# Kernel optimization log

Measured on AMD Instinct MI355X. Metric: run time of the kernel, lower is better.

## Reference

```python
import jax, jax.numpy as jnp
import numpy as np

N0, N1, N2 = 50000, 12500, 3125
E0, E1, E2 = 800000, 200000, 50000
NNZ = 200000          # nonzeros per interpolation matrix (~4 per fine node)
H = 128               # hidden_channels
F = 32                # feat_dim
L = 3                 # layers
DEC_W = 64            # decoder width


def setup_inputs() -> dict:
    key = jax.random.key(0)
    ks = iter(jax.random.split(key, 64))
    f32 = jnp.float32
    d = {}
    # node features per level
    d['x0'] = jax.random.normal(next(ks), (N0, 6), f32)
    d['x1'] = jax.random.normal(next(ks), (N1, 6), f32)
    d['x2'] = jax.random.normal(next(ks), (N2, 6), f32)
    # edge lists per level
    d['edge_index0'] = jax.random.randint(next(ks), (2, E0), 0, N0)
    d['edge_index1'] = jax.random.randint(next(ks), (2, E1), 0, N1)
    d['edge_index2'] = jax.random.randint(next(ks), (2, E2), 0, N2)
    # sparse interpolation matrices A1: [N0,N1], A2: [N0,N2] in COO
    d['A1_rows'] = jax.random.randint(next(ks), (NNZ,), 0, N0)
    d['A1_cols'] = jax.random.randint(next(ks), (NNZ,), 0, N1)
    d['A1_vals'] = jax.random.uniform(next(ks), (NNZ,), f32)
    d['A2_rows'] = jax.random.randint(next(ks), (NNZ,), 0, N0)
    d['A2_cols'] = jax.random.randint(next(ks), (NNZ,), 0, N2)
    d['A2_vals'] = jax.random.uniform(next(ks), (NNZ,), f32)
    # encoder params, stacked over L layers. GraphConv: lin_rel (bias) + lin_root (no bias)
    s = 0.05
    d['enc_c1_Wrel'] = jax.random.normal(next(ks), (L, 6, H), f32) * s
    d['enc_c1_brel'] = jnp.zeros((L, H), f32)
    d['enc_c1_Wroot'] = jax.random.normal(next(ks), (L, 6, H), f32) * s
    d['enc_c2_Wrel'] = jax.random.normal(next(ks), (L, H, H), f32) * s
    d['enc_c2_brel'] = jnp.zeros((L, H), f32)
    d['enc_c2_Wroot'] = jax.random.normal(next(ks), (L, H, H), f32) * s
    d['enc_lin_W'] = jax.random.normal(next(ks), (L, H, 3 * F), f32) * s
    d['enc_lin_b'] = jnp.zeros((L, 3 * F), f32)
    # decoder params (D=1, W=64, in=L*F, out=1), stacked over 3 decoders
    d['dec_W0'] = jax.random.normal(next(ks), (3, L * F, DEC_W), f32) * s
    d['dec_b0'] = jnp.zeros((3, DEC_W), f32)
    d['dec_Wout'] = jax.random.normal(next(ks), (3, DEC_W, 1), f32) * s
    d['dec_bout'] = jnp.zeros((3, 1), f32)
    return d


def _graph_conv(x, src, dst, Wrel, brel, Wroot, n):
    # PyG GraphConv: lin_rel(sum_{j->i} x_j) + lin_root(x_i)
    agg = jax.ops.segment_sum(x[src], dst, num_segments=n)
    return agg @ Wrel + brel + x @ Wroot


def reference(x0, x1, x2, edge_index0, edge_index1, edge_index2,
              A1_rows, A1_cols, A1_vals, A2_rows, A2_cols, A2_vals,
              enc_c1_Wrel, enc_c1_brel, enc_c1_Wroot,
              enc_c2_Wrel, enc_c2_brel, enc_c2_Wroot,
              enc_lin_W, enc_lin_b,
              dec_W0, dec_b0, dec_Wout, dec_bout):
    xs = (x0, x1, x2)
    eis = (edge_index0, edge_index1, edge_index2)

    def enc(i):
        x, ei = xs[i], eis[i]
        n = x.shape[0]
        src, dst = ei[0], ei[1]
        h = jax.nn.relu(_graph_conv(x, src, dst, enc_c1_Wrel[i], enc_c1_brel[i], enc_c1_Wroot[i], n))
        h = jax.nn.relu(_graph_conv(h, src, dst, enc_c2_Wrel[i], enc_c2_brel[i], enc_c2_Wroot[i], n))
        return h @ enc_lin_W[i] + enc_lin_b[i]  # [n, 3*F]

    e0 = enc(0).reshape(N0, 3, F)
    e1 = enc(1)  # [N1, 3F]
    e2 = enc(2)  # [N2, 3F]
    # sparse.mm(A, dense) as gather-scale-scatter
    i1 = jax.ops.segment_sum(A1_vals[:, None] * e1[A1_cols], A1_rows, num_segments=N0).reshape(N0, 3, F)
    i2 = jax.ops.segment_sum(A2_vals[:, None] * e2[A2_cols], A2_rows, num_segments=N0).reshape(N0, 3, F)
    interped = jnp.concatenate([e0, i1, i2], axis=2)  # [N0, 3, L*F]

    def dec(i):
        h = interped[:, i:i + 1, :]                       # [N0, 1, L*F]
        h = jax.nn.elu(h @ dec_W0[i] + dec_b0[i])         # [N0, 1, 64]
        return h @ dec_Wout[i] + dec_bout[i]              # [N0, 1, 1]

    return jnp.concatenate([dec(0), dec(1), dec(2)], axis=1)  # [N0, 3, 1]
```

## Files before the change

### kernel.cpp

```cpp
#include <hip/hip_runtime.h>
#include <math.h>

#define N0 50000
#define N1 12500
#define N2 3125
#define NNZ 200000
#define NE0 800000
#define NE1 200000
#define NE2 50000
#define NT 65625
#define SEG_TOT 165625
#define EDGE_TOT 1050000
#define ITEM_TOT 1450000
#define NBUCK 324
#define SPB 512
#define NBLK 355

typedef __attribute__((ext_vector_type(8))) short short8;
typedef __attribute__((ext_vector_type(8))) unsigned short ushort8;
typedef __attribute__((ext_vector_type(4))) float floatx4;

__device__ inline void split_bf16(float x, unsigned short& hi, unsigned short& lo) {
    unsigned xb = __float_as_uint(x);
    hi = (unsigned short)(xb >> 16);
    float hf = __uint_as_float((unsigned)hi << 16);
    lo = (unsigned short)(__float_as_uint(x - hf) >> 16);
}

__device__ inline void split8(const float* p, short8& hi, short8& lo) {
    float4 u0 = *(const float4*)p;
    float4 u1 = *(const float4*)(p + 4);
    float f[8] = {u0.x, u0.y, u0.z, u0.w, u1.x, u1.y, u1.z, u1.w};
#pragma unroll
    for (int j = 0; j < 8; j++) {
        unsigned short h, l;
        split_bf16(f[j], h, l);
        hi[j] = (short)h; lo[j] = (short)l;
    }
}


__device__ inline int item_seg(int t, const int* __restrict__ ei0,
                               const int* __restrict__ ei1, const int* __restrict__ ei2,
                               const int* __restrict__ A1r, const int* __restrict__ A2r) {
    if (t < NE0) return ei0[NE0 + t];
    if (t < NE0 + NE1) return 50000 + ei1[NE1 + (t - NE0)];
    if (t < EDGE_TOT) return 62500 + ei2[NE2 + (t - (NE0 + NE1))];
    if (t < EDGE_TOT + NNZ) return NT + A1r[t - EDGE_TOT];
    return NT + N0 + A2r[t - (EDGE_TOT + NNZ)];
}

__global__ __launch_bounds__(256) void bin_hist(const int* __restrict__ ei0,
        const int* __restrict__ ei1, const int* __restrict__ ei2,
        const int* __restrict__ A1r, const int* __restrict__ A2r,
        int* __restrict__ hist_g, int* __restrict__ btot) {
    __shared__ int h[NBUCK];
    for (int i = threadIdx.x; i < NBUCK; i += 256) h[i] = 0;
    __syncthreads();
    int base = blockIdx.x * 4096;
#pragma unroll
    for (int q = 0; q < 16; q++) {
        int t = base + q * 256 + threadIdx.x;
        if (t < ITEM_TOT) atomicAdd(&h[item_seg(t, ei0, ei1, ei2, A1r, A2r) >> 9], 1);
    }
    __syncthreads();
    for (int i = threadIdx.x; i < NBUCK; i += 256) {
        int v = h[i];
        hist_g[i * NBLK + blockIdx.x] = v;
        if (v) atomicAdd(&btot[i], v);
    }
}

__global__ void hist_scan(int* __restrict__ hist_g, const int* __restrict__ btot,
                          int* __restrict__ bbase) {
    int b = blockIdx.x, lane = threadIdx.x;
    int s = 0;
    for (int j = lane; j < b; j += 64) s += btot[j];
#pragma unroll
    for (int o = 32; o > 0; o >>= 1) s += __shfl_down(s, o, 64);
    int base = __shfl(s, 0, 64);
    if (lane == 0) {
        bbase[b] = base;
        if (b == NBUCK - 1) bbase[NBUCK] = ITEM_TOT;
    }
    int v[6], ts = 0;
#pragma unroll
    for (int q = 0; q < 6; q++) {
        int i = lane * 6 + q;
        v[q] = (i < NBLK) ? hist_g[b * NBLK + i] : 0;
        ts += v[q];
    }
    int sc = ts;
#pragma unroll
    for (int o = 1; o < 64; o <<= 1) {
        int t2 = __shfl_up(sc, o, 64);
        if (lane >= o) sc += t2;
    }
    int run = base + sc - ts;
#pragma unroll
    for (int q = 0; q < 6; q++) {
        int i = lane * 6 + q;
        if (i < NBLK) hist_g[b * NBLK + i] = run;
        run += v[q];
    }
}

__global__ __launch_bounds__(256) void bin_scatter(const int* __restrict__ ei0,
        const int* __restrict__ ei1, const int* __restrict__ ei2,
        const int* __restrict__ A1r, const int* __restrict__ A1c, const float* __restrict__ A1v,
        const int* __restrict__ A2r, const int* __restrict__ A2c, const float* __restrict__ A2v,
        const int* __restrict__ hist_g, int* __restrict__ bpacked, float* __restrict__ bval) {
    __shared__ int cur[NBUCK];
    for (int i = threadIdx.x; i < NBUCK; i += 256) cur[i] = hist_g[i * NBLK + blockIdx.x];
    __syncthreads();
    int base = blockIdx.x * 4096;
#pragma unroll
    for (int q = 0; q < 16; q++) {
        int t = base + q * 256 + threadIdx.x;
        if (t >= ITEM_TOT) continue;
        int seg, pay;
        float val = 0.f;
        bool isv = false;
        if (t < NE0) { seg = ei0[NE0 + t]; pay = ei0[t]; }
        else if (t < NE0 + NE1) { int e = t - NE0; seg = 50000 + ei1[NE1 + e]; pay = ei1[e]; }
        else if (t < EDGE_TOT) { int e = t - (NE0 + NE1); seg = 62500 + ei2[NE2 + e]; pay = ei2[e]; }
        else if (t < EDGE_TOT + NNZ) { int k = t - EDGE_TOT; seg = NT + A1r[k]; pay = A1c[k]; val = A1v[k]; isv = true; }
        else { int k = t - (EDGE_TOT + NNZ); seg = NT + N0 + A2r[k]; pay = A2c[k]; val = A2v[k]; isv = true; }
        int bk = seg >> 9;
        int p = atomicAdd(&cur[bk], 1);
        bpacked[p] = ((seg - (bk << 9)) << 16) | pay;
        if (isv) bval[p] = val;
    }
}

__global__ __launch_bounds__(256) void bucket_fill(const int* __restrict__ bpacked,
        const float* __restrict__ bval, const int* __restrict__ bbase,
        int* __restrict__ offs, int* __restrict__ csrc, float* __restrict__ cval) {
    __shared__ int cnt[SPB];
    __shared__ int wsum2[4];
    int b = blockIdx.x, tid = threadIdx.x;
    int segbase = b * SPB;
    int seglim = SEG_TOT - segbase;
    if (seglim > SPB) seglim = SPB;
    int ibeg = bbase[b], iend = bbase[b + 1];
    for (int i = tid; i < SPB; i += 256) cnt[i] = 0;
    __syncthreads();
    for (int i = ibeg + tid; i < iend; i += 256)
        atomicAdd(&cnt[bpacked[i] >> 16], 1);
    __syncthreads();
    int lane = tid & 63, wid = tid >> 6;
    int v0 = cnt[tid * 2], v1 = cnt[tid * 2 + 1];
    int ts = v0 + v1, sc = ts;
#pragma unroll
    for (int o = 1; o < 64; o <<= 1) {
        int t2 = __shfl_up(sc, o, 64);
        if (lane >= o) sc += t2;
    }
    if (lane == 63) wsum2[wid] = sc;
    __syncthreads();
    int woff = 0;
    for (int w = 0; w < wid; w++) woff += wsum2[w];
    int ex = ibeg + woff + sc - ts;
    __syncthreads();
    cnt[tid * 2] = ex;
    cnt[tid * 2 + 1] = ex + v0;
    if (tid * 2 < seglim) offs[segbase + tid * 2] = ex;
    if (tid * 2 + 1 < seglim) offs[segbase + tid * 2 + 1] = ex + v0;
    if (b == NBUCK - 1 && tid == 0) offs[SEG_TOT] = ITEM_TOT;
    __syncthreads();
    for (int i = ibeg + tid; i < iend; i += 256) {
        int w2 = bpacked[i];
        int sl = w2 >> 16, pay = w2 & 0xffff;
        int p = atomicAdd(&cnt[sl], 1);
        csrc[p] = pay;
        if (segbase + sl >= NT) cval[p - EDGE_TOT] = bval[i];
    }
}


__device__ inline void acc_u4(uint4 u, float* a) {
    a[0] += __uint_as_float(u.x << 16);
    a[1] += __uint_as_float(u.x & 0xffff0000u);
    a[2] += __uint_as_float(u.y << 16);
    a[3] += __uint_as_float(u.y & 0xffff0000u);
    a[4] += __uint_as_float(u.z << 16);
    a[5] += __uint_as_float(u.z & 0xffff0000u);
    a[6] += __uint_as_float(u.w << 16);
    a[7] += __uint_as_float(u.w & 0xffff0000u);
}

__global__ __launch_bounds__(256) void gatherH_b(const unsigned short* __restrict__ h1hi,
                                                 const int* __restrict__ offs,
                                                 const int* __restrict__ csrc,
                                                 float* __restrict__ agg) {
    int t = blockIdx.x * blockDim.x + threadIdx.x;
    int n = t >> 4, g = t & 15;
    if (n >= NT) return;
    int nb = (n < 50000) ? 0 : (n < 62500 ? 50000 : 62500);
    float a[8] = {};
    int b = offs[n], e = offs[n + 1];
    int j = b;
    for (; j + 3 < e; j += 4) {
        int s0 = csrc[j], s1 = csrc[j + 1], s2 = csrc[j + 2], s3 = csrc[j + 3];
        uint4 u0 = *(const uint4*)(h1hi + (size_t)(nb + s0) * 128 + g * 8);
        uint4 u1 = *(const uint4*)(h1hi + (size_t)(nb + s1) * 128 + g * 8);
        uint4 u2 = *(const uint4*)(h1hi + (size_t)(nb + s2) * 128 + g * 8);
        uint4 u3 = *(const uint4*)(h1hi + (size_t)(nb + s3) * 128 + g * 8);
        acc_u4(u0, a);
        acc_u4(u1, a);
        acc_u4(u2, a);
        acc_u4(u3, a);
    }
    for (; j < e; j++) {
        uint4 u0 = *(const uint4*)(h1hi + (size_t)(nb + csrc[j]) * 128 + g * 8);
        acc_u4(u0, a);
    }
    float* o = agg + (size_t)n * 128 + g * 8;
    *(float4*)o = (float4){a[0], a[1], a[2], a[3]};
    *(float4*)(o + 4) = (float4){a[4], a[5], a[6], a[7]};
}

__global__ __launch_bounds__(256) void interp_b(const float* __restrict__ ecat,
                                                const int* __restrict__ offs,
                                                const int* __restrict__ csrc,
                                                const float* __restrict__ cval,
                                                float* __restrict__ i1, float* __restrict__ i2) {
    int t = blockIdx.x * blockDim.x + threadIdx.x;
    int ng = t / 24, g = t % 24;
    if (ng >= 2 * N0) return;
    int a = (ng >= N0) ? 1 : 0;
    int nl = ng - a * N0;
    const float* e = ecat + (size_t)(a ? 62500 : 50000) * 96;
    float* ob = a ? i2 : i1;
    int seg = NT + ng;
    float4 s = {0.f, 0.f, 0.f, 0.f};
    int b = offs[seg], en = offs[seg + 1];
    int j = b;
    for (; j + 1 < en; j += 2) {
        int c0 = csrc[j], c1 = csrc[j + 1];
        float v0 = cval[j - EDGE_TOT], v1 = cval[j + 1 - EDGE_TOT];
        float4 w0 = ((const float4*)(e + (size_t)c0 * 96))[g];
        float4 w1 = ((const float4*)(e + (size_t)c1 * 96))[g];
        s.x += v0 * w0.x + v1 * w1.x;
        s.y += v0 * w0.y + v1 * w1.y;
        s.z += v0 * w0.z + v1 * w1.z;
        s.w += v0 * w0.w + v1 * w1.w;
    }
    if (j < en) {
        int c0 = csrc[j];
        float v0 = cval[j - EDGE_TOT];
        float4 w0 = ((const float4*)(e + (size_t)c0 * 96))[g];
        s.x += v0 * w0.x; s.y += v0 * w0.y; s.z += v0 * w0.z; s.w += v0 * w0.w;
    }
    ((float4*)(ob + (size_t)nl * 96))[g] = s;
}

__global__ void conv_weights(const float* __restrict__ c2Wrel, const float* __restrict__ c2Wroot,
                             const float* __restrict__ linW, const float* __restrict__ dW0,
                             unsigned short* __restrict__ c2hi, unsigned short* __restrict__ c2lo,
                             unsigned short* __restrict__ lhi, unsigned short* __restrict__ llo,
                             float* __restrict__ decWt, int* __restrict__ btot) {
    int t = blockIdx.x * blockDim.x + threadIdx.x;
    if (t <= NBUCK) btot[t] = 0;
    if (t < 98304) {
        int i = t / 32768, r = t % 32768;
        int n = r / 256, k = r % 256;
        float w = (k < 128) ? c2Wrel[i * 16384 + k * 128 + n]
                            : c2Wroot[i * 16384 + (k - 128) * 128 + n];
        unsigned short hi, lo;
        split_bf16(w, hi, lo);
        c2hi[t] = hi; c2lo[t] = lo;
    } else if (t < 135168) {
        int u = t - 98304;
        int i = u / 12288, r = u % 12288;
        int n = r / 128, k = r % 128;
        unsigned short hi, lo;
        split_bf16(linW[i * 12288 + k * 96 + n], hi, lo);
        lhi[u] = hi; llo[u] = lo;
    } else if (t < 153600) {
        int u = t - 135168;
        int chn = u / 6144, r = u % 6144;
        int col = r / 96, k = r % 96;
        decWt[u] = dW0[chn * 6144 + k * 64 + col];
    }
}

__global__ __launch_bounds__(256) void conv1_b(
        const int* __restrict__ offs, const int* __restrict__ csrc,
        const float* __restrict__ x0, const float* __restrict__ x1,
        const float* __restrict__ x2,
        const float* __restrict__ Wrel, const float* __restrict__ Wroot,
        const float* __restrict__ brel,
        unsigned short* __restrict__ h1hi, unsigned short* __restrict__ h1lo) {
    __shared__ float As[12][65];
    __shared__ float Ws[12][64];
    int bx = blockIdx.x;
    int l, lbk;
    if (bx < 782) { l = 0; lbk = bx; }
    else if (bx < 978) { l = 1; lbk = bx - 782; }
    else { l = 2; lbk = bx - 978; }
    int nb = (l == 0) ? 0 : (l == 1 ? 50000 : 62500);
    int M = (l == 0) ? N0 : (l == 1 ? N1 : N2);
    const float* xl = (l == 0) ? x0 : (l == 1 ? x1 : x2);
    const float* W1 = Wrel + l * 768;
    const float* W2 = Wroot + l * 768;
    const float* bias = brel + l * 128;
    int m0 = lbk * 64, n0 = blockIdx.y * 64;
    int tid = threadIdx.x;

    {
        int row = tid >> 2, sub = tid & 3;
        int m = m0 + row;
        float a6[6] = {};
        if (m < M) {
            int jb = offs[nb + m], je = offs[nb + m + 1];
            for (int j = jb + sub; j < je; j += 4) {
                const float* p = xl + (size_t)csrc[j] * 6;
                a6[0] += p[0]; a6[1] += p[1]; a6[2] += p[2];
                a6[3] += p[3]; a6[4] += p[4]; a6[5] += p[5];
            }
        }
#pragma unroll
        for (int msk = 1; msk < 4; msk <<= 1) {
#pragma unroll
            for (int q = 0; q < 6; q++) a6[q] += __shfl_xor(a6[q], msk, 64);
        }
        if (sub == 0) {
#pragma unroll
            for (int q = 0; q < 6; q++) As[q][row] = (m < M) ? a6[q] : 0.f;
        } else if (sub == 1) {
#pragma unroll
            for (int q = 0; q < 6; q++)
                As[6 + q][row] = (m < M) ? xl[(size_t)m * 6 + q] : 0.f;
        }
    }
    for (int idx = tid; idx < 768; idx += 256) {
        int kk = idx >> 6, nn2 = idx & 63;
        Ws[kk][nn2] = (kk < 6) ? W1[kk * 128 + n0 + nn2] : W2[(kk - 6) * 128 + n0 + nn2];
    }
    __syncthreads();

    int tm = tid >> 4, tn = tid & 15;
    float acc[4][4] = {};
#pragma unroll
    for (int k = 0; k < 12; k++) {
        float av[4], wv[4];
#pragma unroll
        for (int i = 0; i < 4; i++) av[i] = As[k][tm * 4 + i];
#pragma unroll
        for (int j = 0; j < 4; j++) wv[j] = Ws[k][tn * 4 + j];
#pragma unroll
        for (int i = 0; i < 4; i++)
#pragma unroll
            for (int j = 0; j < 4; j++) acc[i][j] += av[i] * wv[j];
    }
#pragma unroll
    for (int i = 0; i < 4; i++) {
        int m = m0 + tm * 4 + i;
        if (m >= M) continue;
        unsigned short hs[4], ls[4];
#pragma unroll
        for (int j = 0; j < 4; j++) {
            float v = fmaxf(acc[i][j] + bias[n0 + tn * 4 + j], 0.f);
            split_bf16(v, hs[j], ls[j]);
        }
        uint2 ph = {(unsigned)hs[0] | ((unsigned)hs[1] << 16),
                    (unsigned)hs[2] | ((unsigned)hs[3] << 16)};
        uint2 pl = {(unsigned)ls[0] | ((unsigned)ls[1] << 16),
                    (unsigned)ls[2] | ((unsigned)ls[3] << 16)};
        size_t off = (size_t)(nb + m) * 128 + n0 + tn * 4;
        *(uint2*)(h1hi + off) = ph;
        *(uint2*)(h1lo + off) = pl;
    }
}

__global__ __launch_bounds__(256) void conv2lin(
        const float* __restrict__ agg,
        const unsigned short* __restrict__ h1hi, const unsigned short* __restrict__ h1lo,
        const unsigned short* __restrict__ c2hi, const unsigned short* __restrict__ c2lo,
        const float* __restrict__ c2b,
        const unsigned short* __restrict__ lnhi, const unsigned short* __restrict__ lnlo,
        const float* __restrict__ lnb, float* __restrict__ ecat) {
    __shared__ unsigned short smem[25088];
    unsigned short* Ah = smem;
    unsigned short* Al = smem + 2560;
    unsigned short* Bh = smem + 5120;
    unsigned short* Bl = smem + 10240;
    unsigned short* Hh = smem;
    unsigned short* Hl = smem + 8704;
    unsigned short* B2h = smem + 17408;
    unsigned short* B2l = smem + 21248;
    const int LDA = 40;

    int bx = blockIdx.x;
    int l, lbk;
    if (bx < 782) { l = 0; lbk = bx; }
    else if (bx < 978) { l = 1; lbk = bx - 782; }
    else { l = 2; lbk = bx - 978; }
    int nb = (l == 0) ? 0 : (l == 1 ? 50000 : 62500);
    int M = (l == 0) ? N0 : (l == 1 ? N1 : N2);
    const float* A1 = agg + (size_t)nb * 128;
    const unsigned short* A2h = h1hi + (size_t)nb * 128;
    const unsigned short* A2l = h1lo + (size_t)nb * 128;
    const unsigned short* W1h = c2hi + l * 32768;
    const unsigned short* W1l = c2lo + l * 32768;
    const float* b1 = c2b + l * 128;
    const unsigned short* W2h = lnhi + l * 12288;
    const unsigned short* W2l = lnlo + l * 12288;
    const float* b2 = lnb + l * 96;
    float* C = ecat + (size_t)nb * 96;
    int m0 = lbk * 64;

    int tid = threadIdx.x;
    int lane = tid & 63, wid = tid >> 6;
    int waveM = wid & 1, waveN = wid >> 1;
    int l15 = lane & 15, quad = lane >> 4;
    int arow = tid >> 2, acol = (tid & 3) * 8;
    int brow = tid >> 1, bcol = (tid & 1) * 16;

    floatx4 acc[2][4];
#pragma unroll
    for (int i = 0; i < 2; i++)
#pragma unroll
        for (int j = 0; j < 4; j++) acc[i][j] = (floatx4){0.f, 0.f, 0.f, 0.f};

    for (int kt = 0; kt < 256; kt += 32) {
        __syncthreads();
        {
            int m = m0 + arow;
            ushort8 hv, lv;
            if (m < M) {
                int kg = kt + acol;
                if (kg < 128) {
                    const float* src = A1 + (size_t)m * 128 + kg;
                    float4 u0 = *(const float4*)src;
                    float4 u1 = *(const float4*)(src + 4);
                    float xv[8] = {u0.x, u0.y, u0.z, u0.w, u1.x, u1.y, u1.z, u1.w};
#pragma unroll
                    for (int q = 0; q < 8; q++) {
                        unsigned short h, lo2;
                        split_bf16(xv[q], h, lo2);
                        hv[q] = h; lv[q] = lo2;
                    }
                } else {
                    size_t off = (size_t)m * 128 + (kg - 128);
                    hv = *(const ushort8*)(A2h + off);
                    lv = *(const ushort8*)(A2l + off);
                }
            } else {
                hv = (ushort8)0; lv = (ushort8)0;
            }
            *(ushort8*)(&Ah[arow * LDA + acol]) = hv;
            *(ushort8*)(&Al[arow * LDA + acol]) = lv;
        }
        {
            const unsigned short* ph = W1h + (size_t)brow * 256 + kt + bcol;
            const unsigned short* pl = W1l + (size_t)brow * 256 + kt + bcol;
            *(ushort8*)(&Bh[brow * LDA + bcol]) = *(const ushort8*)ph;
            *(ushort8*)(&Bh[brow * LDA + bcol + 8]) = *(const ushort8*)(ph + 8);
            *(ushort8*)(&Bl[brow * LDA + bcol]) = *(const ushort8*)pl;
            *(ushort8*)(&Bl[brow * LDA + bcol + 8]) = *(const ushort8*)(pl + 8);
        }
        __syncthreads();
        short8 af[2][2];
#pragma unroll
        for (int mt = 0; mt < 2; mt++) {
            int r = waveM * 32 + mt * 16 + l15;
            af[mt][0] = *(const short8*)(&Ah[r * LDA + quad * 8]);
            af[mt][1] = *(const short8*)(&Al[r * LDA + quad * 8]);
        }
#pragma unroll
        for (int nt = 0; nt < 4; nt++) {
            int c = waveN * 64 + nt * 16 + l15;
            short8 bh = *(const short8*)(&Bh[c * LDA + quad * 8]);
            short8 bl = *(const short8*)(&Bl[c * LDA + quad * 8]);
#pragma unroll
            for (int mt = 0; mt < 2; mt++) {
                acc[mt][nt] = __builtin_amdgcn_mfma_f32_16x16x32_bf16(af[mt][0], bh, acc[mt][nt], 0, 0, 0);
                acc[mt][nt] = __builtin_amdgcn_mfma_f32_16x16x32_bf16(af[mt][0], bl, acc[mt][nt], 0, 0, 0);
                acc[mt][nt] = __builtin_amdgcn_mfma_f32_16x16x32_bf16(af[mt][1], bh, acc[mt][nt], 0, 0, 0);
            }
        }
    }

    __syncthreads();
    {
        float bs1[4];
#pragma unroll
        for (int nt = 0; nt < 4; nt++) bs1[nt] = b1[waveN * 64 + nt * 16 + l15];
#pragma unroll
        for (int mt = 0; mt < 2; mt++)
#pragma unroll
            for (int nt = 0; nt < 4; nt++)
#pragma unroll
                for (int r = 0; r < 4; r++) {
                    int row = waveM * 32 + mt * 16 + quad * 4 + r;
                    int col = waveN * 64 + nt * 16 + l15;
                    float v = fmaxf(acc[mt][nt][r] + bs1[nt], 0.f);
                    unsigned short h, lo2;
                    split_bf16(v, h, lo2);
                    Hh[row * 136 + col] = h;
                    Hl[row * 136 + col] = lo2;
                }
    }

    floatx4 acc2[2][3];
#pragma unroll
    for (int i = 0; i < 2; i++)
#pragma unroll
        for (int j = 0; j < 3; j++) acc2[i][j] = (floatx4){0.f, 0.f, 0.f, 0.f};

    for (int kt = 0; kt < 128; kt += 32) {
        __syncthreads();
        if (brow < 96) {
            const unsigned short* ph = W2h + (size_t)brow * 128 + kt + bcol;
            const unsigned short* pl = W2l + (size_t)brow * 128 + kt + bcol;
            *(ushort8*)(&B2h[brow * LDA + bcol]) = *(const ushort8*)ph;
            *(ushort8*)(&B2h[brow * LDA + bcol + 8]) = *(const ushort8*)(ph + 8);
            *(ushort8*)(&B2l[brow * LDA + bcol]) = *(const ushort8*)pl;
            *(ushort8*)(&B2l[brow * LDA + bcol + 8]) = *(const ushort8*)(pl + 8);
        }
        __syncthreads();
        short8 af2[2][2];
#pragma unroll
        for (int mt = 0; mt < 2; mt++) {
            int r = waveM * 32 + mt * 16 + l15;
            af2[mt][0] = *(const short8*)(&Hh[r * 136 + kt + quad * 8]);
            af2[mt][1] = *(const short8*)(&Hl[r * 136 + kt + quad * 8]);
        }
#pragma unroll
        for (int nt = 0; nt < 3; nt++) {
            int c = waveN * 48 + nt * 16 + l15;
            short8 bh = *(const short8*)(&B2h[c * LDA + quad * 8]);
            short8 bl = *(const short8*)(&B2l[c * LDA + quad * 8]);
#pragma unroll
            for (int mt = 0; mt < 2; mt++) {
                acc2[mt][nt] = __builtin_amdgcn_mfma_f32_16x16x32_bf16(af2[mt][0], bh, acc2[mt][nt], 0, 0, 0);
                acc2[mt][nt] = __builtin_amdgcn_mfma_f32_16x16x32_bf16(af2[mt][0], bl, acc2[mt][nt], 0, 0, 0);
                acc2[mt][nt] = __builtin_amdgcn_mfma_f32_16x16x32_bf16(af2[mt][1], bh, acc2[mt][nt], 0, 0, 0);
            }
        }
    }

    float bs2[3];
#pragma unroll
    for (int nt = 0; nt < 3; nt++) bs2[nt] = b2[waveN * 48 + nt * 16 + l15];
#pragma unroll
    for (int mt = 0; mt < 2; mt++)
#pragma unroll
        for (int r = 0; r < 4; r++) {
            int grow = m0 + waveM * 32 + mt * 16 + quad * 4 + r;
            if (grow >= M) continue;
#pragma unroll
            for (int nt = 0; nt < 3; nt++) {
                int col = waveN * 48 + nt * 16 + l15;
                C[(size_t)grow * 96 + col] = acc2[mt][nt][r] + bs2[nt];
            }
        }
}

__global__ __launch_bounds__(256) void decoder_mfma(
        const float* __restrict__ e0, const float* __restrict__ i1,
        const float* __restrict__ i2, const float* __restrict__ decWt,
        const float* __restrict__ b0, const float* __restrict__ Wout,
        const float* __restrict__ bout, float* __restrict__ out, int N) {
    __shared__ float As[6400];
    __shared__ float Bs[6400];
    __shared__ float red[64][2];
    __shared__ float sb0[64], sWo[64];
    int ch = blockIdx.y;
    int tid = threadIdx.x;
    int m0 = blockIdx.x * 64;

    for (int idx = tid; idx < 1536; idx += 256) {
        int col = idx / 24, k0 = (idx % 24) * 4;
        *(float4*)(&Bs[col * 100 + k0]) = *(const float4*)(decWt + ch * 6144 + col * 96 + k0);
    }
    if (tid < 64) { sb0[tid] = b0[ch * 64 + tid]; sWo[tid] = Wout[ch * 64 + tid]; }
    for (int idx = tid; idx < 1536; idx += 256) {
        int row = idx / 24, k0 = (idx % 24) * 4;
        int m = m0 + row;
        float4 v = {0.f, 0.f, 0.f, 0.f};
        if (m < N) {
            const float* base = (k0 < 32) ? e0 : (k0 < 64 ? i1 : i2);
            v = *(const float4*)(base + (size_t)m * 96 + ch * 32 + (k0 & 31));
        }
        *(float4*)(&As[row * 100 + k0]) = v;
    }
    __syncthreads();

    int lane = tid & 63, wid = tid >> 6;
    int waveM = wid & 1, waveN = wid >> 1;
    int l15 = lane & 15, quad = lane >> 4;
    floatx4 acc[2][2];
#pragma unroll
    for (int i = 0; i < 2; i++)
#pragma unroll
        for (int j = 0; j < 2; j++) acc[i][j] = (floatx4){0.f, 0.f, 0.f, 0.f};

#pragma unroll
    for (int kt = 0; kt < 96; kt += 32) {
        short8 ah[2], al[2];
#pragma unroll
        for (int mt = 0; mt < 2; mt++) {
            int r = waveM * 32 + mt * 16 + l15;
            split8(&As[r * 100 + kt + quad * 8], ah[mt], al[mt]);
        }
#pragma unroll
        for (int nt = 0; nt < 2; nt++) {
            int c = waveN * 32 + nt * 16 + l15;
            short8 bh, bl;
            split8(&Bs[c * 100 + kt + quad * 8], bh, bl);
#pragma unroll
            for (int mt = 0; mt < 2; mt++) {
                acc[mt][nt] = __builtin_amdgcn_mfma_f32_16x16x32_bf16(ah[mt], bh, acc[mt][nt], 0, 0, 0);
                acc[mt][nt] = __builtin_amdgcn_mfma_f32_16x16x32_bf16(ah[mt], bl, acc[mt][nt], 0, 0, 0);
                acc[mt][nt] = __builtin_amdgcn_mfma_f32_16x16x32_bf16(al[mt], bh, acc[mt][nt], 0, 0, 0);
            }
        }
    }

    float cb0[2], cwo[2];
#pragma unroll
    for (int nt = 0; nt < 2; nt++) {
        int col = waveN * 32 + nt * 16 + l15;
        cb0[nt] = sb0[col]; cwo[nt] = sWo[col];
    }
    float p[2][4];
#pragma unroll
    for (int mt = 0; mt < 2; mt++)
#pragma unroll
        for (int r = 0; r < 4; r++) {
            float s = 0.f;
#pragma unroll
            for (int nt = 0; nt < 2; nt++) {
                float h = acc[mt][nt][r] + cb0[nt];
                h = h > 0.f ? h : (expf(h) - 1.0f);
                s += h * cwo[nt];
            }
            p[mt][r] = s;
        }
#pragma unroll
    for (int mt = 0; mt < 2; mt++)
#pragma unroll
        for (int r = 0; r < 4; r++) {
#pragma unroll
            for (int msk = 1; msk < 16; msk <<= 1)
                p[mt][r] += __shfl_xor(p[mt][r], msk, 64);
        }
    if (l15 == 0) {
#pragma unroll
        for (int mt = 0; mt < 2; mt++)
#pragma unroll
            for (int r = 0; r < 4; r++) {
                int row = waveM * 32 + mt * 16 + quad * 4 + r;
                red[row][waveN] = p[mt][r];
            }
    }
    __syncthreads();
    if (tid < 64) {
        int m = m0 + tid;
        if (m < N) out[(size_t)m * 3 + ch] = red[tid][0] + red[tid][1] + bout[ch];
    }
}


extern "C" void kernel_launch(void* const* d_in, const int* in_sizes, int n_in,
                              void* d_out, int out_size, void* d_ws, size_t ws_size,
                              hipStream_t stream) {
    const float* x0 = (const float*)d_in[0];
    const float* x1 = (const float*)d_in[1];
    const float* x2 = (const float*)d_in[2];
    const int* ei0 = (const int*)d_in[3];
    const int* ei1 = (const int*)d_in[4];
    const int* ei2 = (const int*)d_in[5];
    const int* A1r = (const int*)d_in[6];
    const int* A1c = (const int*)d_in[7];
    const float* A1v = (const float*)d_in[8];
    const int* A2r = (const int*)d_in[9];
    const int* A2c = (const int*)d_in[10];
    const float* A2v = (const float*)d_in[11];
    const float* c1Wrel = (const float*)d_in[12];
    const float* c1brel = (const float*)d_in[13];
    const float* c1Wroot = (const float*)d_in[14];
    const float* c2Wrel = (const float*)d_in[15];
    const float* c2brel = (const float*)d_in[16];
    const float* c2Wroot = (const float*)d_in[17];
    const float* linW = (const float*)d_in[18];
    const float* linb = (const float*)d_in[19];
    const float* dW0 = (const float*)d_in[20];
    const float* db0 = (const float*)d_in[21];
    const float* dWout = (const float*)d_in[22];
    const float* dbout = (const float*)d_in[23];
    float* out = (float*)d_out;

    float* ws = (float*)d_ws;
    unsigned short* h1hi = (unsigned short*)(ws + 400000);
    unsigned short* h1lo = (unsigned short*)(ws + 4600000);
    float* aggH = ws + 8800000;
    float* ecat = ws + 17200000;
    int* bpacked = (int*)(ws + 8800000);
    float* bval = ws + 8800000 + 1450000;
    float* i1 = aggH;
    float* i2 = ws + 400000;
    int* hist_g = (int*)(ws + 23500000);
    int* btot = (int*)(ws + 23615020);
    int* bbase = (int*)(ws + 23615344);
    int* offs = (int*)(ws + 23665632);
    int* csrc = (int*)(ws + 23831264);
    float* cval = ws + 25281392;
    unsigned short* c2hi = (unsigned short*)(ws + 25681392);
    unsigned short* c2lo = c2hi + 98304;
    unsigned short* lnhi = c2lo + 98304;
    unsigned short* lnlo = lnhi + 36864;
    float* decWt = ws + 25681392 + 135168;

    conv_weights<<<(153600 + 255) / 256, 256, 0, stream>>>(
        c2Wrel, c2Wroot, linW, dW0, c2hi, c2lo, lnhi, lnlo, decWt, btot);

    bin_hist<<<NBLK, 256, 0, stream>>>(ei0, ei1, ei2, A1r, A2r, hist_g, btot);
    hist_scan<<<NBUCK, 64, 0, stream>>>(hist_g, btot, bbase);
    bin_scatter<<<NBLK, 256, 0, stream>>>(ei0, ei1, ei2, A1r, A1c, A1v,
                                          A2r, A2c, A2v, hist_g, bpacked, bval);
    bucket_fill<<<NBUCK, 256, 0, stream>>>(bpacked, bval, bbase, offs, csrc, cval);

    dim3 g1(1027, 2);
    conv1_b<<<g1, 256, 0, stream>>>(offs, csrc, x0, x1, x2,
                                    c1Wrel, c1Wroot, c1brel, h1hi, h1lo);
    gatherH_b<<<((size_t)NT * 16 + 255) / 256, 256, 0, stream>>>(h1hi, offs, csrc, aggH);
    conv2lin<<<1027, 256, 0, stream>>>(aggH, h1hi, h1lo, c2hi, c2lo, c2brel,
                                       lnhi, lnlo, linb, ecat);

    interp_b<<<((size_t)2 * N0 * 24 + 255) / 256, 256, 0, stream>>>(
        ecat, offs, csrc, cval, i1, i2);

    dim3 gd(782, 3);
    decoder_mfma<<<gd, 256, 0, stream>>>(ecat, i1, i2, decWt, db0, dWout, dbout, out, N0);
}
```

Measured before the change: 306.5 us.

## Store aggregated conv2 input as single bf16 and merge conv1 column blocks

The neighbor aggregate of conv1 output is now written as round-to-nearest bf16 instead of fp32. This halves its write and read traffic, and conv2lin drops the lo-part split and its MFMA for the first half of K. conv1_b now computes all 128 output columns per block instead of launching two column blocks, so the neighbor gather of x runs once rather than twice. Workspace offsets are shuffled so the bucket buffers no longer alias the aggregate. The trade is reduced precision on the aggregated term of the second conv.

```diff
diff --git a/kernel.cpp b/kernel.cpp
--- a/kernel.cpp
+++ b/kernel.cpp
@@ -25,6 +25,11 @@
     hi = (unsigned short)(xb >> 16);
     float hf = __uint_as_float((unsigned)hi << 16);
     lo = (unsigned short)(__float_as_uint(x - hf) >> 16);
+}
+
+__device__ inline unsigned short bf16_rne(float x) {
+    unsigned xb = __float_as_uint(x);
+    return (unsigned short)((xb + 0x7fff + ((xb >> 16) & 1)) >> 16);
 }
 
 __device__ inline void split8(const float* p, short8& hi, short8& lo) {
@@ -192,7 +197,7 @@
 __global__ __launch_bounds__(256) void gatherH_b(const unsigned short* __restrict__ h1hi,
                                                  const int* __restrict__ offs,
                                                  const int* __restrict__ csrc,
-                                                 float* __restrict__ agg) {
+                                                 unsigned short* __restrict__ aggh) {
     int t = blockIdx.x * blockDim.x + threadIdx.x;
     int n = t >> 4, g = t & 15;
     if (n >= NT) return;
@@ -215,9 +220,10 @@
         uint4 u0 = *(const uint4*)(h1hi + (size_t)(nb + csrc[j]) * 128 + g * 8);
         acc_u4(u0, a);
     }
-    float* o = agg + (size_t)n * 128 + g * 8;
-    *(float4*)o = (float4){a[0], a[1], a[2], a[3]};
-    *(float4*)(o + 4) = (float4){a[4], a[5], a[6], a[7]};
+    ushort8 o;
+#pragma unroll
+    for (int q = 0; q < 8; q++) o[q] = bf16_rne(a[q]);
+    *(ushort8*)(aggh + (size_t)n * 128 + g * 8) = o;
 }
 
 __global__ __launch_bounds__(256) void interp_b(const float* __restrict__ ecat,
@@ -293,7 +299,7 @@
         const float* __restrict__ brel,
         unsigned short* __restrict__ h1hi, unsigned short* __restrict__ h1lo) {
     __shared__ float As[12][65];
-    __shared__ float Ws[12][64];
+    __shared__ float Ws[12][128];
     int bx = blockIdx.x;
     int l, lbk;
     if (bx < 782) { l = 0; lbk = bx; }
@@ -305,7 +311,7 @@
     const float* W1 = Wrel + l * 768;
     const float* W2 = Wroot + l * 768;
     const float* bias = brel + l * 128;
-    int m0 = lbk * 64, n0 = blockIdx.y * 64;
+    int m0 = lbk * 64;
     int tid = threadIdx.x;
 
     {
@@ -334,48 +340,52 @@
                 As[6 + q][row] = (m < M) ? xl[(size_t)m * 6 + q] : 0.f;
         }
     }
-    for (int idx = tid; idx < 768; idx += 256) {
-        int kk = idx >> 6, nn2 = idx & 63;
-        Ws[kk][nn2] = (kk < 6) ? W1[kk * 128 + n0 + nn2] : W2[(kk - 6) * 128 + n0 + nn2];
+    for (int idx = tid; idx < 1536; idx += 256) {
+        int kk = idx >> 7, nn2 = idx & 127;
+        Ws[kk][nn2] = (kk < 6) ? W1[kk * 128 + nn2] : W2[(kk - 6) * 128 + nn2];
     }
     __syncthreads();
 
     int tm = tid >> 4, tn = tid & 15;
-    float acc[4][4] = {};
+    float acc[4][8] = {};
 #pragma unroll
     for (int k = 0; k < 12; k++) {
-        float av[4], wv[4];
+        float av[4], wv[8];
 #pragma unroll
         for (int i = 0; i < 4; i++) av[i] = As[k][tm * 4 + i];
 #pragma unroll
-        for (int j = 0; j < 4; j++) wv[j] = Ws[k][tn * 4 + j];
+        for (int j = 0; j < 4; j++) { wv[j] = Ws[k][tn * 4 + j]; wv[4 + j] = Ws[k][64 + tn * 4 + j]; }
 #pragma unroll
         for (int i = 0; i < 4; i++)
 #pragma unroll
-            for (int j = 0; j < 4; j++) acc[i][j] += av[i] * wv[j];
+            for (int j = 0; j < 8; j++) acc[i][j] += av[i] * wv[j];
     }
 #pragma unroll
     for (int i = 0; i < 4; i++) {
         int m = m0 + tm * 4 + i;
         if (m >= M) continue;
-        unsigned short hs[4], ls[4];
-#pragma unroll
-        for (int j = 0; j < 4; j++) {
-            float v = fmaxf(acc[i][j] + bias[n0 + tn * 4 + j], 0.f);
-            split_bf16(v, hs[j], ls[j]);
-        }
-        uint2 ph = {(unsigned)hs[0] | ((unsigned)hs[1] << 16),
-                    (unsigned)hs[2] | ((unsigned)hs[3] << 16)};
-        uint2 pl = {(unsigned)ls[0] | ((unsigned)ls[1] << 16),
-                    (unsigned)ls[2] | ((unsigned)ls[3] << 16)};
-        size_t off = (size_t)(nb + m) * 128 + n0 + tn * 4;
-        *(uint2*)(h1hi + off) = ph;
-        *(uint2*)(h1lo + off) = pl;
+#pragma unroll
+        for (int half = 0; half < 2; half++) {
+            int c0 = half * 64 + tn * 4;
+            unsigned short hs[4], ls[4];
+#pragma unroll
+            for (int j = 0; j < 4; j++) {
+                float v = fmaxf(acc[i][half * 4 + j] + bias[c0 + j], 0.f);
+                split_bf16(v, hs[j], ls[j]);
+            }
+            uint2 ph = {(unsigned)hs[0] | ((unsigned)hs[1] << 16),
+                        (unsigned)hs[2] | ((unsigned)hs[3] << 16)};
+            uint2 pl = {(unsigned)ls[0] | ((unsigned)ls[1] << 16),
+                        (unsigned)ls[2] | ((unsigned)ls[3] << 16)};
+            size_t off = (size_t)(nb + m) * 128 + c0;
+            *(uint2*)(h1hi + off) = ph;
+            *(uint2*)(h1lo + off) = pl;
+        }
     }
 }
 
 __global__ __launch_bounds__(256) void conv2lin(
-        const float* __restrict__ agg,
+        const unsigned short* __restrict__ aggh,
         const unsigned short* __restrict__ h1hi, const unsigned short* __restrict__ h1lo,
         const unsigned short* __restrict__ c2hi, const unsigned short* __restrict__ c2lo,
         const float* __restrict__ c2b,
@@ -399,7 +409,7 @@
     else { l = 2; lbk = bx - 978; }
     int nb = (l == 0) ? 0 : (l == 1 ? 50000 : 62500);
     int M = (l == 0) ? N0 : (l == 1 ? N1 : N2);
-    const float* A1 = agg + (size_t)nb * 128;
+    const unsigned short* A1h = aggh + (size_t)nb * 128;
     const unsigned short* A2h = h1hi + (size_t)nb * 128;
     const unsigned short* A2l = h1lo + (size_t)nb * 128;
     const unsigned short* W1h = c2hi + l * 32768;
@@ -425,33 +435,23 @@
         for (int j = 0; j < 4; j++) acc[i][j] = (floatx4){0.f, 0.f, 0.f, 0.f};
 
     for (int kt = 0; kt < 256; kt += 32) {
+        bool hasLo = (kt >= 128);
         __syncthreads();
         {
             int m = m0 + arow;
-            ushort8 hv, lv;
+            ushort8 hv = (ushort8)0, lv = (ushort8)0;
             if (m < M) {
                 int kg = kt + acol;
-                if (kg < 128) {
-                    const float* src = A1 + (size_t)m * 128 + kg;
-                    float4 u0 = *(const float4*)src;
-                    float4 u1 = *(const float4*)(src + 4);
-                    float xv[8] = {u0.x, u0.y, u0.z, u0.w, u1.x, u1.y, u1.z, u1.w};
-#pragma unroll
-                    for (int q = 0; q < 8; q++) {
-                        unsigned short h, lo2;
-                        split_bf16(xv[q], h, lo2);
-                        hv[q] = h; lv[q] = lo2;
-                    }
+                if (!hasLo) {
+                    hv = *(const ushort8*)(A1h + (size_t)m * 128 + kg);
                 } else {
                     size_t off = (size_t)m * 128 + (kg - 128);
                     hv = *(const ushort8*)(A2h + off);
                     lv = *(const ushort8*)(A2l + off);
                 }
-            } else {
-                hv = (ushort8)0; lv = (ushort8)0;
             }
             *(ushort8*)(&Ah[arow * LDA + acol]) = hv;
-            *(ushort8*)(&Al[arow * LDA + acol]) = lv;
+            if (hasLo) *(ushort8*)(&Al[arow * LDA + acol]) = lv;
         }
         {
             const unsigned short* ph = W1h + (size_t)brow * 256 + kt + bcol;
@@ -467,7 +467,7 @@
         for (int mt = 0; mt < 2; mt++) {
             int r = waveM * 32 + mt * 16 + l15;
             af[mt][0] = *(const short8*)(&Ah[r * LDA + quad * 8]);
-            af[mt][1] = *(const short8*)(&Al[r * LDA + quad * 8]);
+            if (hasLo) af[mt][1] = *(const short8*)(&Al[r * LDA + quad * 8]);
         }
 #pragma unroll
         for (int nt = 0; nt < 4; nt++) {
@@ -478,7 +478,8 @@
             for (int mt = 0; mt < 2; mt++) {
                 acc[mt][nt] = __builtin_amdgcn_mfma_f32_16x16x32_bf16(af[mt][0], bh, acc[mt][nt], 0, 0, 0);
                 acc[mt][nt] = __builtin_amdgcn_mfma_f32_16x16x32_bf16(af[mt][0], bl, acc[mt][nt], 0, 0, 0);
-                acc[mt][nt] = __builtin_amdgcn_mfma_f32_16x16x32_bf16(af[mt][1], bh, acc[mt][nt], 0, 0, 0);
+                if (hasLo)
+                    acc[mt][nt] = __builtin_amdgcn_mfma_f32_16x16x32_bf16(af[mt][1], bh, acc[mt][nt], 0, 0, 0);
             }
         }
     }
@@ -697,11 +698,11 @@
     float* ws = (float*)d_ws;
     unsigned short* h1hi = (unsigned short*)(ws + 400000);
     unsigned short* h1lo = (unsigned short*)(ws + 4600000);
-    float* aggH = ws + 8800000;
+    unsigned short* aggh = (unsigned short*)(ws + 8800000);
     float* ecat = ws + 17200000;
-    int* bpacked = (int*)(ws + 8800000);
-    float* bval = ws + 8800000 + 1450000;
-    float* i1 = aggH;
+    int* bpacked = (int*)(ws + 13000000);
+    float* bval = ws + 13000000 + 1450000;
+    float* i1 = ws + 8800000;
     float* i2 = ws + 400000;
     int* hist_g = (int*)(ws + 23500000);
     int* btot = (int*)(ws + 23615020);
@@ -724,11 +725,10 @@
                                           A2r, A2c, A2v, hist_g, bpacked, bval);
     bucket_fill<<<NBUCK, 256, 0, stream>>>(bpacked, bval, bbase, offs, csrc, cval);
 
-    dim3 g1(1027, 2);
-    conv1_b<<<g1, 256, 0, stream>>>(offs, csrc, x0, x1, x2,
-                                    c1Wrel, c1Wroot, c1brel, h1hi, h1lo);
-    gatherH_b<<<((size_t)NT * 16 + 255) / 256, 256, 0, stream>>>(h1hi, offs, csrc, aggH);
-    conv2lin<<<1027, 256, 0, stream>>>(aggH, h1hi, h1lo, c2hi, c2lo, c2brel,
+    conv1_b<<<1027, 256, 0, stream>>>(offs, csrc, x0, x1, x2,
+                                      c1Wrel, c1Wroot, c1brel, h1hi, h1lo);
+    gatherH_b<<<((size_t)NT * 16 + 255) / 256, 256, 0, stream>>>(h1hi, offs, csrc, aggh);
+    conv2lin<<<1027, 256, 0, stream>>>(aggh, h1hi, h1lo, c2hi, c2lo, c2brel,
                                        lnhi, lnlo, linb, ecat);
 
     interp_b<<<((size_t)2 * N0 * 24 + 255) / 256, 256, 0, stream>>>(
```

Measured after the change: 298.4 us. 1.03x faster.
